# Kernel optimization log

Measured on AMD Instinct MI355X. Metric: run time of the kernel, lower is better.

The kernel has to match this reference:

```python
import math
import jax, jax.numpy as jnp
import numpy as np

D_MODEL = 1024
N_HEADS = 16
D_K = D_MODEL // N_HEADS


def _build_neighbours(n_heads):
    # Mirrors LatticeMultiHeadAttention._build_neighbours for a (4,4)-style lattice.
    side = int(math.sqrt(n_heads))
    cols = side + 1 if side * side < n_heads else side
    positions = [divmod(i, cols) for i in range(n_heads)]
    pos_map = {p: j for j, p in enumerate(positions)}
    nb_idx = np.full((n_heads, 8), -1, dtype=np.int64)
    nb_w = np.zeros((n_heads, 8), dtype=np.float32)
    for i, (r, c) in enumerate(positions):
        k = 0
        for dr in (-1, 0, 1):
            for dc in (-1, 0, 1):
                if dr == 0 and dc == 0:
                    continue
                j = pos_map.get((r + dr, c + dc))
                if j is not None and k < 8:
                    nb_idx[i, k] = j
                    nb_w[i, k] = math.exp(-math.hypot(dr, dc))
                    k += 1
    return nb_idx, nb_w


def _phase_biases(coupling):
    # Sequential Kuramoto phase update: head h uses neighbor phases already
    # updated for heads < h (exactly as the torch per-head loop mutates buffers).
    H = coupling.shape[0]
    nb_idx, nb_w = _build_neighbours(H)
    phases = [jnp.asarray(0.0, coupling.dtype) for _ in range(H)]
    two_pi = 2.0 * math.pi
    for h in range(H):
        force = jnp.asarray(0.0, coupling.dtype)
        for k in range(8):
            j = int(nb_idx[h, k])
            if j >= 0:
                force = force + jnp.asarray(nb_w[h, k], coupling.dtype) * jnp.sin(phases[j] - phases[h])
        intrinsic = 1.0 + 0.1 * h
        new_phase = (phases[h] + 0.01 * (intrinsic + coupling[h] * force)) % two_pi
        phases[h] = new_phase
    return 0.1 * jnp.cos(jnp.stack(phases))  # [H] per-head scalar bias


def setup_inputs() -> dict:
    key = jax.random.key(0)
    ks = jax.random.split(key, 9)
    B, L = 2, 2048
    std = 0.02
    return {
        "query": jax.random.normal(ks[0], (B, L, D_MODEL), jnp.float32),
        "key": jax.random.normal(ks[1], (B, L, D_MODEL), jnp.float32),
        "value": jax.random.normal(ks[2], (B, L, D_MODEL), jnp.float32),
        "Wq": std * jax.random.normal(ks[3], (N_HEADS, D_MODEL, D_K), jnp.float32),
        "Wk": std * jax.random.normal(ks[4], (N_HEADS, D_MODEL, D_K), jnp.float32),
        "Wv": std * jax.random.normal(ks[5], (N_HEADS, D_MODEL, D_K), jnp.float32),
        "out_w": std * jax.random.normal(ks[6], (D_MODEL, D_MODEL), jnp.float32),
        "out_b": jnp.zeros((D_MODEL,), jnp.float32),
        "coupling": 0.1 * jnp.ones((N_HEADS,), jnp.float32),
    }


def reference(query, key, value, Wq, Wk, Wv, out_w, out_b, coupling):
    d_k = Wq.shape[-1]
    Q = jnp.einsum("bld,hdk->bhlk", query, Wq)
    K = jnp.einsum("bld,hdk->bhlk", key, Wk)
    V = jnp.einsum("bld,hdk->bhlk", value, Wv)
    scale = jnp.asarray(math.sqrt(float(d_k)), query.dtype)
    scores = jnp.einsum("bhlk,bhmk->bhlm", Q, K) / scale
    bias = _phase_biases(coupling)  # [H]
    scores = scores + bias[None, :, None, None]
    attn = jax.nn.softmax(scores, axis=-1)
    ctx = jnp.einsum("bhlm,bhmk->bhlk", attn, V)
    B, H, L, _ = ctx.shape
    out = ctx.transpose(0, 2, 1, 3).reshape(B, L, H * d_k)  # concat heads
    return out @ out_w + out_b
```

## Files before the change

### kernel.cpp

```cpp
#include <hip/hip_runtime.h>
#include <cstdint>

typedef uint16_t u16;
typedef __attribute__((ext_vector_type(8))) short bf16x8;
typedef __attribute__((ext_vector_type(4))) float f32x4;
typedef __attribute__((ext_vector_type(16))) float f32x16;

#define QSCALE 0.18033688011112042f

struct Ptr3 { const float* a; const float* b; const float* c; };

__device__ __forceinline__ u16 f2bf(float x) {
  union { float f; uint32_t u; } v; v.f = x;
  uint32_t r = (v.u + 0x7fffu + ((v.u >> 16) & 1u)) >> 16;
  return (u16)r;
}

#if __has_builtin(__builtin_amdgcn_cvt_pk_bf16_f32)
typedef __bf16 bf2_t __attribute__((ext_vector_type(2)));
__device__ __forceinline__ uint32_t pkbf(float a, float b) {
  bf2_t v = __builtin_amdgcn_cvt_pk_bf16_f32(a, b);
  uint32_t u;
  __builtin_memcpy(&u, &v, 4);
  return u;
}
#else
__device__ __forceinline__ uint32_t pkbf(float a, float b) {
  return (uint32_t)f2bf(a) | ((uint32_t)f2bf(b) << 16);
}
#endif

#if __has_builtin(__builtin_amdgcn_permlane32_swap)
typedef __attribute__((ext_vector_type(2))) int i32x2;
__device__ __forceinline__ void swap32(uint32_t& a, uint32_t& b, int hi) {
  i32x2 r = __builtin_amdgcn_permlane32_swap((int)a, (int)b, false, false);
  a = (uint32_t)r.x;
  b = (uint32_t)r.y;
}
#else
__device__ __forceinline__ void swap32(uint32_t& a, uint32_t& b, int hi) {
  uint32_t ax = (uint32_t)__shfl_xor((int)a, 32);
  uint32_t bx = (uint32_t)__shfl_xor((int)b, 32);
  uint32_t na = hi ? bx : a;
  uint32_t nb = hi ? b : ax;
  a = na; b = nb;
}
#endif

__device__ __forceinline__ void async16(void* lds, const void* g) {
  __builtin_amdgcn_global_load_lds((const __attribute__((address_space(1))) void*)g,
                                   (__attribute__((address_space(3))) void*)lds, 16, 0, 0);
}

__global__ __launch_bounds__(256) void k_prep(Ptr3 in, u16* __restrict__ out,
                                              Ptr3 w, const float* __restrict__ ow,
                                              u16* __restrict__ wt, u16* __restrict__ wto) {
  __shared__ u16 tile[64 * 65];
  const int t = threadIdx.x;
  const int bx = blockIdx.x;
  if (bx < 12288) {
    int z = bx >> 12;
    int i = (bx & 4095) * 256 + t;
    const float* p = z == 0 ? in.a : (z == 1 ? in.b : in.c);
    float4 v = ((const float4*)p)[i];
    uint2 o2;
    o2.x = pkbf(v.x, v.y);
    o2.y = pkbf(v.z, v.w);
    *(uint2*)(out + (long)z * 4194304 + (long)i * 4) = o2;
    return;
  }
  const int b2 = bx - 12288;
  const float* src;
  long in_base, out_base;
  int rstr, r0, c0;
  u16* outp;
  if (b2 < 768) {
    int z = b2 >> 4;
    r0 = (b2 & 15) * 64; c0 = 0;
    src = (z < 16) ? w.a : (z < 32 ? w.b : w.c);
    in_base = (long)(z & 15) * 65536;
    out_base = (long)z * 65536;
    rstr = 64; outp = wt;
  } else {
    int idx = b2 - 768;
    r0 = (idx >> 4) * 64; c0 = (idx & 15) * 64;
    src = ow; in_base = 0; out_base = 0;
    rstr = 1024; outp = wto;
  }
  for (int e = t; e < 4096; e += 256) {
    int rr = e >> 6, cc = e & 63;
    tile[rr * 65 + cc] = f2bf(src[in_base + (long)(r0 + rr) * rstr + c0 + cc]);
  }
  __syncthreads();
  for (int s = t; s < 512; s += 256) {
    int cc = s >> 3, r8 = (s & 7) << 3;
    bf16x8 p;
    #pragma unroll
    for (int j = 0; j < 8; ++j) p[j] = (short)tile[(r8 + j) * 65 + cc];
    *(bf16x8*)(outp + out_base + (long)(c0 + cc) * 1024 + r0 + r8) = p;
  }
}

__global__ __launch_bounds__(256) void k_gemm_qkv(const u16* __restrict__ A0,
                                                  const u16* __restrict__ B0,
                                                  u16* __restrict__ C0,
                                                  u16* __restrict__ Vt, float scale0) {
  __shared__ __align__(16) u16 smem[16640];
  u16* As = smem;
  u16* Bs = smem + 8192;
  u16* T  = smem;
  const int z = blockIdx.z;
  const u16* A = A0 + (long)z * 4194304;
  const u16* Bt = B0 + (long)z * 1048576;
  const int t = threadIdx.x, lane = t & 63, quad = lane >> 4, l16 = lane & 15;
  const int wave = t >> 6, wy = wave >> 1, wx = wave & 1;
  const int m0 = blockIdx.x * 128, n0 = blockIdx.y * 128;
  const int wbase = t & 192;
  f32x4 acc[4][4] = {};
  for (int k0 = 0; k0 < 1024; k0 += 64) {
    __syncthreads();
    #pragma unroll
    for (int i = 0; i < 4; ++i) {
      int sb = i * 256 + wbase;
      int s = sb + lane;
      int row = s >> 3, c = s & 7;
      int cs = c ^ (row & 7);
      async16(As + sb * 8, A + (long)(m0 + row) * 1024 + k0 + cs * 8);
      async16(Bs + sb * 8, Bt + (long)(n0 + row) * 1024 + k0 + cs * 8);
    }
    __syncthreads();
    #pragma unroll
    for (int kk = 0; kk < 2; ++kk) {
      bf16x8 af[4], bfr[4];
      #pragma unroll
      for (int mt = 0; mt < 4; ++mt) {
        int row = wy * 64 + mt * 16 + l16;
        int pos = (kk * 4 + quad) ^ (row & 7);
        af[mt] = *(const bf16x8*)(As + row * 64 + pos * 8);
      }
      #pragma unroll
      for (int nt = 0; nt < 4; ++nt) {
        int row = wx * 64 + nt * 16 + l16;
        int pos = (kk * 4 + quad) ^ (row & 7);
        bfr[nt] = *(const bf16x8*)(Bs + row * 64 + pos * 8);
      }
      #pragma unroll
      for (int mt = 0; mt < 4; ++mt)
        #pragma unroll
        for (int nt = 0; nt < 4; ++nt)
          acc[mt][nt] = __builtin_amdgcn_mfma_f32_16x16x32_bf16(af[mt], bfr[nt], acc[mt][nt], 0, 0, 0);
    }
  }
  if (z < 2) {
    u16* C = C0 + (long)z * 4194304;
    const float scale = z ? 1.0f : scale0;
    #pragma unroll
    for (int mt = 0; mt < 4; ++mt)
      #pragma unroll
      for (int nt = 0; nt < 4; ++nt) {
        int col = n0 + wx * 64 + nt * 16 + l16;
        int row = m0 + wy * 64 + mt * 16 + quad * 4;
        uint32_t ua = pkbf(acc[mt][nt][0] * scale, acc[mt][nt][1] * scale);
        uint32_t ub = pkbf(acc[mt][nt][2] * scale, acc[mt][nt][3] * scale);
        C[(long)row * 1024 + col] = (u16)ua;
        C[(long)(row + 1) * 1024 + col] = (u16)(ua >> 16);
        C[(long)(row + 2) * 1024 + col] = (u16)ub;
        C[(long)(row + 3) * 1024 + col] = (u16)(ub >> 16);
      }
  } else {
    __syncthreads();
    #pragma unroll
    for (int mt = 0; mt < 4; ++mt)
      #pragma unroll
      for (int nt = 0; nt < 4; ++nt) {
        int cc = wx * 64 + nt * 16 + l16;
        int rr = wy * 64 + mt * 16 + quad * 4;
        uint32_t ua = pkbf(acc[mt][nt][0], acc[mt][nt][1]);
        uint32_t ub = pkbf(acc[mt][nt][2], acc[mt][nt][3]);
        T[(rr + 0) * 130 + cc] = (u16)ua;
        T[(rr + 1) * 130 + cc] = (u16)(ua >> 16);
        T[(rr + 2) * 130 + cc] = (u16)ub;
        T[(rr + 3) * 130 + cc] = (u16)(ub >> 16);
      }
    __syncthreads();
    const int h0 = blockIdx.y * 2, bb = m0 >> 11, lb = m0 & 2047;
    #pragma unroll
    for (int i = 0; i < 8; ++i) {
      int s = t + i * 256;
      int c = s >> 4, l0 = (s & 15) * 8;
      bf16x8 p;
      #pragma unroll
      for (int j = 0; j < 8; ++j) p[j] = (short)T[(l0 + j) * 130 + c];
      *(bf16x8*)(Vt + (long)(bb * 16 + h0 + (c >> 6)) * 131072 +
                 (long)(c & 63) * 2048 + lb + l0) = p;
    }
  }
}

__global__ __launch_bounds__(256) void k_gemm_out(const u16* __restrict__ A,
                                                  const u16* __restrict__ Bt,
                                                  float* __restrict__ C,
                                                  const float* __restrict__ bias) {
  __shared__ __align__(16) u16 As[128 * 32];
  __shared__ __align__(16) u16 Bs[64 * 32];
  const int t = threadIdx.x, lane = t & 63, quad = lane >> 4, l16 = lane & 15;
  const int wave = t >> 6;
  const int m0 = blockIdx.x * 128, n0 = blockIdx.y * 64;
  const int wbase = t & 192;
  f32x4 acc[2][4] = {};
  for (int k0 = 0; k0 < 1024; k0 += 32) {
    __syncthreads();
    #pragma unroll
    for (int i = 0; i < 2; ++i) {
      int sb = i * 256 + wbase;
      int s = sb + lane;
      int row = s >> 2, c = s & 3;
      async16(As + sb * 8, A + (long)(m0 + row) * 1024 + k0 + c * 8);
    }
    {
      int s = t;
      int row = s >> 2, c = s & 3;
      async16(Bs + wbase * 8, Bt + (long)(n0 + row) * 1024 + k0 + c * 8);
    }
    __syncthreads();
    bf16x8 af[2], bfr[4];
    #pragma unroll
    for (int mt = 0; mt < 2; ++mt)
      af[mt] = *(const bf16x8*)(As + (wave * 32 + mt * 16 + l16) * 32 + quad * 8);
    #pragma unroll
    for (int nt = 0; nt < 4; ++nt)
      bfr[nt] = *(const bf16x8*)(Bs + (nt * 16 + l16) * 32 + quad * 8);
    #pragma unroll
    for (int mt = 0; mt < 2; ++mt)
      #pragma unroll
      for (int nt = 0; nt < 4; ++nt)
        acc[mt][nt] = __builtin_amdgcn_mfma_f32_16x16x32_bf16(af[mt], bfr[nt], acc[mt][nt], 0, 0, 0);
  }
  #pragma unroll
  for (int mt = 0; mt < 2; ++mt)
    #pragma unroll
    for (int nt = 0; nt < 4; ++nt) {
      int col = n0 + nt * 16 + l16;
      #pragma unroll
      for (int r = 0; r < 4; ++r) {
        int row = m0 + wave * 32 + mt * 16 + quad * 4 + r;
        C[(long)row * 1024 + col] = acc[mt][nt][r] + bias[col];
      }
    }
}

__global__ __launch_bounds__(512, 2) void k_flash(const u16* __restrict__ Qp,
                                                  const u16* __restrict__ Kp,
                                                  const u16* __restrict__ Vt,
                                                  u16* __restrict__ ctx) {
  __shared__ __align__(16) u16 qs[256 * 64];
  __shared__ __align__(16) u16 ks[64 * 72];
  __shared__ __align__(16) u16 vs[64 * 72];
  const int t = threadIdx.x, lane = t & 63, hi = lane >> 5, l32 = lane & 31;
  const int wave = t >> 6;
  const int bh = blockIdx.x & 31, b = bh >> 4, h = bh & 15;
  const int q0 = (blockIdx.x >> 5) * 256;
  const long gkbase = (long)b * 2097152 + h * 64;
  const long gvbase = (long)bh * 131072;
  const int srow = t >> 3, sc = t & 7;

  {
    long gq = (long)(b * 2048 + q0) * 1024 + h * 64;
    #pragma unroll
    for (int i = 0; i < 4; ++i) {
      int s = i * 512 + t;
      int row = s >> 3, pos = s & 7, c = pos ^ (row & 7);
      async16(qs + (long)s * 8, Qp + gq + (long)row * 1024 + c * 8);
    }
  }
  bf16x8 kreg = *(const bf16x8*)(Kp + gkbase + (long)srow * 1024 + sc * 8);
  bf16x8 vreg = *(const bf16x8*)(Vt + gvbase + (long)srow * 2048 + sc * 8);
  __syncthreads();

  bf16x8 qf[4];
  {
    int m = wave * 32 + l32;
    #pragma unroll
    for (int sd = 0; sd < 4; ++sd) {
      int pos = (sd * 2 + hi) ^ (m & 7);
      qf[sd] = *(const bf16x8*)(qs + m * 64 + pos * 8);
    }
  }
  *(bf16x8*)(ks + srow * 72 + sc * 8) = kreg;
  *(bf16x8*)(vs + srow * 72 + sc * 8) = vreg;
  __syncthreads();

  const short one_bf = (short)0x3F80;
  const bf16x8 ones = {one_bf, one_bf, one_bf, one_bf,
                       one_bf, one_bf, one_bf, one_bf};

  f32x16 o0 = {}, o1 = {};
  f32x16 ol = {};

  for (int kt = 0; kt < 32; ++kt) {
    if (kt < 31) {
      int kv0 = (kt + 1) * 64;
      kreg = *(const bf16x8*)(Kp + gkbase + (long)(kv0 + srow) * 1024 + sc * 8);
      vreg = *(const bf16x8*)(Vt + gvbase + kv0 + (long)srow * 2048 + sc * 8);
    }

    bf16x8 kf0[4], kf1[4], vf0[4], vf1[4];
    #pragma unroll
    for (int sd = 0; sd < 4; ++sd) {
      kf0[sd] = *(const bf16x8*)(ks + (l32) * 72 + sd * 16 + hi * 8);
      kf1[sd] = *(const bf16x8*)(ks + (32 + l32) * 72 + sd * 16 + hi * 8);
      vf0[sd] = *(const bf16x8*)(vs + (l32) * 72 + sd * 16 + hi * 8);
      vf1[sd] = *(const bf16x8*)(vs + (32 + l32) * 72 + sd * 16 + hi * 8);
    }

    f32x16 p0 = {}, p1 = {};
    __builtin_amdgcn_s_setprio(1);
    #pragma unroll
    for (int sd = 0; sd < 4; ++sd) {
      p0 = __builtin_amdgcn_mfma_f32_32x32x16_bf16(kf0[sd], qf[sd], p0, 0, 0, 0);
      p1 = __builtin_amdgcn_mfma_f32_32x32x16_bf16(kf1[sd], qf[sd], p1, 0, 0, 0);
    }
    __builtin_amdgcn_s_setprio(0);
    #pragma unroll
    for (int r = 0; r < 16; ++r) {
      p0[r] = __builtin_amdgcn_exp2f(p0[r]);
      p1[r] = __builtin_amdgcn_exp2f(p1[r]);
    }
    #pragma unroll
    for (int s = 0; s < 4; ++s) {
      const int oct = (s & 1) * 8;
      uint32_t xA, yA, xB, yB;
      if (s < 2) {
        xA = pkbf(p0[oct + 0], p0[oct + 1]);
        yA = pkbf(p0[oct + 2], p0[oct + 3]);
        xB = pkbf(p0[oct + 4], p0[oct + 5]);
        yB = pkbf(p0[oct + 6], p0[oct + 7]);
      } else {
        xA = pkbf(p1[oct + 0], p1[oct + 1]);
        yA = pkbf(p1[oct + 2], p1[oct + 3]);
        xB = pkbf(p1[oct + 4], p1[oct + 5]);
        yB = pkbf(p1[oct + 6], p1[oct + 7]);
      }
      swap32(xA, xB, hi);
      swap32(yA, yB, hi);
      union { uint32_t w[4]; bf16x8 v; } pa;
      pa.w[0] = xA; pa.w[1] = yA; pa.w[2] = xB; pa.w[3] = yB;
      __builtin_amdgcn_s_setprio(1);
      o0 = __builtin_amdgcn_mfma_f32_32x32x16_bf16(pa.v, vf0[s], o0, 0, 0, 0);
      o1 = __builtin_amdgcn_mfma_f32_32x32x16_bf16(pa.v, vf1[s], o1, 0, 0, 0);
      ol = __builtin_amdgcn_mfma_f32_32x32x16_bf16(pa.v, ones, ol, 0, 0, 0);
      __builtin_amdgcn_s_setprio(0);
    }

    __syncthreads();
    if (kt < 31) {
      *(bf16x8*)(ks + srow * 72 + sc * 8) = kreg;
      *(bf16x8*)(vs + srow * 72 + sc * 8) = vreg;
    }
    __syncthreads();
  }

  #pragma unroll
  for (int r = 0; r < 16; r += 2) {
    float li0 = 1.0f / ol[r];
    float li1 = 1.0f / ol[r + 1];
    int q = q0 + wave * 32 + (r & 3) + 8 * (r >> 2) + 4 * hi;
    long idx = (long)(b * 2048 + q) * 1024 + h * 64 + l32;
    uint32_t u0 = pkbf(o0[r] * li0, o0[r + 1] * li1);
    uint32_t u1 = pkbf(o1[r] * li0, o1[r + 1] * li1);
    ctx[idx]             = (u16)u0;
    ctx[idx + 1024]      = (u16)(u0 >> 16);
    ctx[idx + 32]        = (u16)u1;
    ctx[idx + 32 + 1024] = (u16)(u1 >> 16);
  }
}

extern "C" void kernel_launch(void* const* d_in, const int* in_sizes, int n_in,
                              void* d_out, int out_size, void* d_ws, size_t ws_size,
                              hipStream_t stream) {
  const float* query = (const float*)d_in[0];
  const float* key   = (const float*)d_in[1];
  const float* value = (const float*)d_in[2];
  const float* Wq    = (const float*)d_in[3];
  const float* Wk    = (const float*)d_in[4];
  const float* Wv    = (const float*)d_in[5];
  const float* out_w = (const float*)d_in[6];
  const float* out_b = (const float*)d_in[7];
  float* out = (float*)d_out;

  char* ws = (char*)d_ws;
  size_t off = 0;
  auto alloc = [&](size_t bytes) {
    void* p = ws + off;
    off += (bytes + 255) & ~(size_t)255;
    return p;
  };
  u16* qb  = (u16*)alloc(4096L * 1024 * 2);
  u16* kb  = (u16*)alloc(4096L * 1024 * 2);
  u16* vb  = (u16*)alloc(4096L * 1024 * 2);
  u16* wtq = (u16*)alloc(1024L * 1024 * 2);
  u16* wtk = (u16*)alloc(1024L * 1024 * 2);
  u16* wtv = (u16*)alloc(1024L * 1024 * 2);
  u16* wto = (u16*)alloc(1024L * 1024 * 2);
  u16* Qp  = (u16*)alloc(4096L * 1024 * 2);
  u16* Kp  = (u16*)alloc(4096L * 1024 * 2);
  u16* Vtb = (u16*)alloc(4096L * 1024 * 2);
  u16* ctx = qb;
  (void)kb; (void)vb; (void)wtk; (void)wtv; (void)Kp;

  k_prep<<<13312, 256, 0, stream>>>(Ptr3{query, key, value}, qb,
                                    Ptr3{Wq, Wk, Wv}, out_w, wtq, wto);

  k_gemm_qkv<<<dim3(32, 8, 3), 256, 0, stream>>>(qb, wtq, Qp, Vtb, QSCALE);

  k_flash<<<256, 512, 0, stream>>>(Qp, Kp, Vtb, ctx);

  k_gemm_out<<<dim3(32, 16), 256, 0, stream>>>(ctx, wto, out, out_b);
}
```

Before: 218.5 us.

## Double KV tile to 128 rows and load Q fragments directly from global

```diff
diff --git a/kernel.cpp b/kernel.cpp
--- a/kernel.cpp
+++ b/kernel.cpp
@@ -253,9 +253,8 @@
                                                   const u16* __restrict__ Kp,
                                                   const u16* __restrict__ Vt,
                                                   u16* __restrict__ ctx) {
-  __shared__ __align__(16) u16 qs[256 * 64];
-  __shared__ __align__(16) u16 ks[64 * 72];
-  __shared__ __align__(16) u16 vs[64 * 72];
+  __shared__ __align__(16) u16 ks[128 * 72];
+  __shared__ __align__(16) u16 vs[64 * 136];
   const int t = threadIdx.x, lane = t & 63, hi = lane >> 5, l32 = lane & 31;
   const int wave = t >> 6;
   const int bh = blockIdx.x & 31, b = bh >> 4, h = bh & 15;
@@ -264,30 +263,23 @@
   const long gvbase = (long)bh * 131072;
   const int srow = t >> 3, sc = t & 7;
 
-  {
-    long gq = (long)(b * 2048 + q0) * 1024 + h * 64;
-    #pragma unroll
-    for (int i = 0; i < 4; ++i) {
-      int s = i * 512 + t;
-      int row = s >> 3, pos = s & 7, c = pos ^ (row & 7);
-      async16(qs + (long)s * 8, Qp + gq + (long)row * 1024 + c * 8);
-    }
-  }
-  bf16x8 kreg = *(const bf16x8*)(Kp + gkbase + (long)srow * 1024 + sc * 8);
-  bf16x8 vreg = *(const bf16x8*)(Vt + gvbase + (long)srow * 2048 + sc * 8);
-  __syncthreads();
-
   bf16x8 qf[4];
   {
-    int m = wave * 32 + l32;
-    #pragma unroll
-    for (int sd = 0; sd < 4; ++sd) {
-      int pos = (sd * 2 + hi) ^ (m & 7);
-      qf[sd] = *(const bf16x8*)(qs + m * 64 + pos * 8);
-    }
-  }
-  *(bf16x8*)(ks + srow * 72 + sc * 8) = kreg;
-  *(bf16x8*)(vs + srow * 72 + sc * 8) = vreg;
+    long gq = (long)(b * 2048 + q0 + wave * 32 + l32) * 1024 + h * 64;
+    #pragma unroll
+    for (int sd = 0; sd < 4; ++sd)
+      qf[sd] = *(const bf16x8*)(Qp + gq + sd * 16 + hi * 8);
+  }
+  {
+    bf16x8 k0 = *(const bf16x8*)(Kp + gkbase + (long)srow * 1024 + sc * 8);
+    bf16x8 k1 = *(const bf16x8*)(Kp + gkbase + (long)(srow + 64) * 1024 + sc * 8);
+    bf16x8 v0 = *(const bf16x8*)(Vt + gvbase + (long)srow * 2048 + sc * 8);
+    bf16x8 v1 = *(const bf16x8*)(Vt + gvbase + 64 + (long)srow * 2048 + sc * 8);
+    *(bf16x8*)(ks + srow * 72 + sc * 8) = k0;
+    *(bf16x8*)(ks + (srow + 64) * 72 + sc * 8) = k1;
+    *(bf16x8*)(vs + srow * 136 + sc * 8) = v0;
+    *(bf16x8*)(vs + srow * 136 + 64 + sc * 8) = v1;
+  }
   __syncthreads();
 
   const short one_bf = (short)0x3F80;
@@ -296,66 +288,75 @@
 
   f32x16 o0 = {}, o1 = {};
   f32x16 ol = {};
-
-  for (int kt = 0; kt < 32; ++kt) {
-    if (kt < 31) {
-      int kv0 = (kt + 1) * 64;
-      kreg = *(const bf16x8*)(Kp + gkbase + (long)(kv0 + srow) * 1024 + sc * 8);
-      vreg = *(const bf16x8*)(Vt + gvbase + kv0 + (long)srow * 2048 + sc * 8);
-    }
-
-    bf16x8 kf0[4], kf1[4], vf0[4], vf1[4];
-    #pragma unroll
-    for (int sd = 0; sd < 4; ++sd) {
-      kf0[sd] = *(const bf16x8*)(ks + (l32) * 72 + sd * 16 + hi * 8);
-      kf1[sd] = *(const bf16x8*)(ks + (32 + l32) * 72 + sd * 16 + hi * 8);
-      vf0[sd] = *(const bf16x8*)(vs + (l32) * 72 + sd * 16 + hi * 8);
-      vf1[sd] = *(const bf16x8*)(vs + (32 + l32) * 72 + sd * 16 + hi * 8);
-    }
-
-    f32x16 p0 = {}, p1 = {};
-    __builtin_amdgcn_s_setprio(1);
-    #pragma unroll
-    for (int sd = 0; sd < 4; ++sd) {
-      p0 = __builtin_amdgcn_mfma_f32_32x32x16_bf16(kf0[sd], qf[sd], p0, 0, 0, 0);
-      p1 = __builtin_amdgcn_mfma_f32_32x32x16_bf16(kf1[sd], qf[sd], p1, 0, 0, 0);
-    }
-    __builtin_amdgcn_s_setprio(0);
-    #pragma unroll
-    for (int r = 0; r < 16; ++r) {
-      p0[r] = __builtin_amdgcn_exp2f(p0[r]);
-      p1[r] = __builtin_amdgcn_exp2f(p1[r]);
-    }
-    #pragma unroll
-    for (int s = 0; s < 4; ++s) {
-      const int oct = (s & 1) * 8;
-      uint32_t xA, yA, xB, yB;
-      if (s < 2) {
-        xA = pkbf(p0[oct + 0], p0[oct + 1]);
-        yA = pkbf(p0[oct + 2], p0[oct + 3]);
-        xB = pkbf(p0[oct + 4], p0[oct + 5]);
-        yB = pkbf(p0[oct + 6], p0[oct + 7]);
-      } else {
-        xA = pkbf(p1[oct + 0], p1[oct + 1]);
-        yA = pkbf(p1[oct + 2], p1[oct + 3]);
-        xB = pkbf(p1[oct + 4], p1[oct + 5]);
-        yB = pkbf(p1[oct + 6], p1[oct + 7]);
-      }
-      swap32(xA, xB, hi);
-      swap32(yA, yB, hi);
-      union { uint32_t w[4]; bf16x8 v; } pa;
-      pa.w[0] = xA; pa.w[1] = yA; pa.w[2] = xB; pa.w[3] = yB;
+  bf16x8 kreg0, kreg1, vreg0, vreg1;
+
+  for (int kt = 0; kt < 16; ++kt) {
+    if (kt < 15) {
+      int kv0 = (kt + 1) * 128;
+      kreg0 = *(const bf16x8*)(Kp + gkbase + (long)(kv0 + srow) * 1024 + sc * 8);
+      kreg1 = *(const bf16x8*)(Kp + gkbase + (long)(kv0 + srow + 64) * 1024 + sc * 8);
+      vreg0 = *(const bf16x8*)(Vt + gvbase + kv0 + (long)srow * 2048 + sc * 8);
+      vreg1 = *(const bf16x8*)(Vt + gvbase + kv0 + 64 + (long)srow * 2048 + sc * 8);
+    }
+
+    #pragma unroll
+    for (int hb = 0; hb < 2; ++hb) {
+      const int kvb = hb * 64;
+      bf16x8 kf0[4], kf1[4], vf0[4], vf1[4];
+      #pragma unroll
+      for (int sd = 0; sd < 4; ++sd) {
+        kf0[sd] = *(const bf16x8*)(ks + (kvb + l32) * 72 + sd * 16 + hi * 8);
+        kf1[sd] = *(const bf16x8*)(ks + (kvb + 32 + l32) * 72 + sd * 16 + hi * 8);
+        vf0[sd] = *(const bf16x8*)(vs + (l32) * 136 + kvb + sd * 16 + hi * 8);
+        vf1[sd] = *(const bf16x8*)(vs + (32 + l32) * 136 + kvb + sd * 16 + hi * 8);
+      }
+
+      f32x16 p0 = {}, p1 = {};
       __builtin_amdgcn_s_setprio(1);
-      o0 = __builtin_amdgcn_mfma_f32_32x32x16_bf16(pa.v, vf0[s], o0, 0, 0, 0);
-      o1 = __builtin_amdgcn_mfma_f32_32x32x16_bf16(pa.v, vf1[s], o1, 0, 0, 0);
-      ol = __builtin_amdgcn_mfma_f32_32x32x16_bf16(pa.v, ones, ol, 0, 0, 0);
+      #pragma unroll
+      for (int sd = 0; sd < 4; ++sd) {
+        p0 = __builtin_amdgcn_mfma_f32_32x32x16_bf16(kf0[sd], qf[sd], p0, 0, 0, 0);
+        p1 = __builtin_amdgcn_mfma_f32_32x32x16_bf16(kf1[sd], qf[sd], p1, 0, 0, 0);
+      }
       __builtin_amdgcn_s_setprio(0);
-    }
-
-    __syncthreads();
-    if (kt < 31) {
-      *(bf16x8*)(ks + srow * 72 + sc * 8) = kreg;
-      *(bf16x8*)(vs + srow * 72 + sc * 8) = vreg;
+      #pragma unroll
+      for (int r = 0; r < 16; ++r) {
+        p0[r] = __builtin_amdgcn_exp2f(p0[r]);
+        p1[r] = __builtin_amdgcn_exp2f(p1[r]);
+      }
+      #pragma unroll
+      for (int s = 0; s < 4; ++s) {
+        const int oct = (s & 1) * 8;
+        uint32_t xA, yA, xB, yB;
+        if (s < 2) {
+          xA = pkbf(p0[oct + 0], p0[oct + 1]);
+          yA = pkbf(p0[oct + 2], p0[oct + 3]);
+          xB = pkbf(p0[oct + 4], p0[oct + 5]);
+          yB = pkbf(p0[oct + 6], p0[oct + 7]);
+        } else {
+          xA = pkbf(p1[oct + 0], p1[oct + 1]);
+          yA = pkbf(p1[oct + 2], p1[oct + 3]);
+          xB = pkbf(p1[oct + 4], p1[oct + 5]);
+          yB = pkbf(p1[oct + 6], p1[oct + 7]);
+        }
+        swap32(xA, xB, hi);
+        swap32(yA, yB, hi);
+        union { uint32_t w[4]; bf16x8 v; } pa;
+        pa.w[0] = xA; pa.w[1] = yA; pa.w[2] = xB; pa.w[3] = yB;
+        __builtin_amdgcn_s_setprio(1);
+        o0 = __builtin_amdgcn_mfma_f32_32x32x16_bf16(pa.v, vf0[s], o0, 0, 0, 0);
+        o1 = __builtin_amdgcn_mfma_f32_32x32x16_bf16(pa.v, vf1[s], o1, 0, 0, 0);
+        ol = __builtin_amdgcn_mfma_f32_32x32x16_bf16(pa.v, ones, ol, 0, 0, 0);
+        __builtin_amdgcn_s_setprio(0);
+      }
+    }
+
+    __syncthreads();
+    if (kt < 15) {
+      *(bf16x8*)(ks + srow * 72 + sc * 8) = kreg0;
+      *(bf16x8*)(ks + (srow + 64) * 72 + sc * 8) = kreg1;
+      *(bf16x8*)(vs + srow * 136 + sc * 8) = vreg0;
+      *(bf16x8*)(vs + srow * 136 + 64 + sc * 8) = vreg1;
     }
     __syncthreads();
   }
```

Measured after the change: 221.6 us. About the same (+1.4%).
